# Kernel optimization log

Hardware: AMD Instinct MI355X
Metric: run time of the kernel (lower is better)

Reference implementation:

```python
import jax, jax.numpy as jnp
import numpy as np

N, IN_F, OUT_F, H = 4096, 128, 64, 8


def setup_inputs() -> dict:
    key = jax.random.key(0)
    k1, k2, k3, k4 = jax.random.split(key, 4)
    input_A = jax.random.normal(k1, (N, IN_F), jnp.float32)
    # linear_proj.weight: [H*OUT_F, IN_F] (torch Linear convention), xavier-ish scale
    Wp = jax.random.normal(k2, (H * OUT_F, IN_F), jnp.float32) * (1.0 / np.sqrt(IN_F))
    a_src = jax.random.normal(k3, (H, OUT_F), jnp.float32) * 0.1
    a_tgt = jax.random.normal(k4, (H, OUT_F), jnp.float32) * 0.1
    # dense additive mask (0 = connected); zeros => fully-connected graph, same math path
    adj_mask = jnp.zeros((N, N), jnp.float32)
    return {"input_A": input_A, "adj_mask": adj_mask, "Wp": Wp, "a_src": a_src, "a_tgt": a_tgt}


def reference(input_A, adj_mask, Wp, a_src, a_tgt):
    # dropout is identity in eval mode
    xp = (input_A @ Wp.T).reshape(-1, H, OUT_F)          # [N, H, F]
    ss = jnp.einsum('nhf,hf->hn', xp, a_src)             # scores_source, [H, N]
    st = jnp.einsum('nhf,hf->hn', xp, a_tgt)             # scores_target, [H, N]
    scores = jax.nn.leaky_relu(ss[:, :, None] + st[:, None, :], negative_slope=0.2)  # [H, N, N]
    attn = jax.nn.softmax(scores + adj_mask[None, :, :], axis=-1)                    # [H, N, N]
    out = jnp.einsum('hnm,mhf->nhf', attn, xp)           # bmm aggregate, [N, H, F]
    out = out.mean(axis=1)                               # mean over heads, [N, F]
    return jax.nn.relu(out)
```

## Files before the change

kernel.cpp:

```cpp
#include <hip/hip_runtime.h>
#include <hip/hip_bf16.h>
#include <cstdint>

#define GN 4096
#define GIN 128
#define GF 64
#define GH 8
#define GHF (GH*GF)
#define LOG2E 1.4426950408889634f

typedef __attribute__((ext_vector_type(8))) short short8v;
typedef __attribute__((ext_vector_type(4))) float f32x4;

__device__ __forceinline__ short f2bf(float x) {
    uint32_t u = __float_as_uint(x);
    uint32_t r = u + 0x7fffu + ((u >> 16) & 1u);
    return (short)(r >> 16);
}
__device__ __forceinline__ uint32_t pack_bf16_rh(float lo, float hi) {
    uint32_t a = __float_as_uint(lo) + 0x8000u;
    uint32_t b = __float_as_uint(hi) + 0x8000u;
    return __builtin_amdgcn_perm(b, a, 0x07060302u);
}
__device__ __forceinline__ float leaky(float t) { return fmaxf(t, 0.2f * t); }

__global__ void gat_zeroflag(uint32_t* __restrict__ f) {
    if (threadIdx.x == 0 && blockIdx.x == 0) f[0] = 0u;
}
__global__ __launch_bounds__(256) void gat_maskscan(const uint32_t* __restrict__ m,
                                                    uint32_t* __restrict__ flag) {
    uint32_t acc = 0;
    const uint4* m4 = (const uint4*)m;
    const int total = (GN * GN) / 4;
    for (int i = blockIdx.x * 256 + threadIdx.x; i < total; i += gridDim.x * 256) {
        uint4 v = m4[i];
        acc |= v.x | v.y | v.z | v.w;
    }
#pragma unroll
    for (int d = 1; d < 64; d <<= 1) acc |= (uint32_t)__shfl_xor((int)acc, d);
    __shared__ uint32_t wred[4];
    if ((threadIdx.x & 63) == 0) wred[threadIdx.x >> 6] = acc;
    __syncthreads();
    if (threadIdx.x == 0) {
        uint32_t a = wred[0] | wred[1] | wred[2] | wred[3];
        if (a) atomicOr(flag, 1u);
    }
}

__global__ __launch_bounds__(256) void gat_proj(const float* __restrict__ A,
                                                const float* __restrict__ W,
                                                const float* __restrict__ a_src,
                                                const float* __restrict__ a_tgt,
                                                float* __restrict__ ss,
                                                float* __restrict__ st,
                                                short* __restrict__ bh) {
    __shared__ float lds[2 * 64 * 129];
    float* As = lds;
    float* Ws = lds + 64 * 129;
    const int n0 = blockIdx.x * 64;
    const int h  = blockIdx.y;
    const int j0 = h * 64;
    const int tid = threadIdx.x;
    const float4* A4 = (const float4*)A;
    const float4* W4 = (const float4*)W;
#pragma unroll
    for (int i = 0; i < 8; ++i) {
        int idx = tid + i * 256;
        int r = idx >> 5, c4 = idx & 31;
        float4 v = A4[(size_t)(n0 + r) * 32 + c4];
        As[r * 129 + c4 * 4 + 0] = v.x; As[r * 129 + c4 * 4 + 1] = v.y;
        As[r * 129 + c4 * 4 + 2] = v.z; As[r * 129 + c4 * 4 + 3] = v.w;
        float4 w = W4[(size_t)(j0 + r) * 32 + c4];
        Ws[r * 129 + c4 * 4 + 0] = w.x; Ws[r * 129 + c4 * 4 + 1] = w.y;
        Ws[r * 129 + c4 * 4 + 2] = w.z; Ws[r * 129 + c4 * 4 + 3] = w.w;
    }
    __syncthreads();
    const int tx = tid & 15, ty = tid >> 4;
    float acc[4][4] = {};
    for (int k = 0; k < 128; ++k) {
        float a[4], b[4];
#pragma unroll
        for (int i = 0; i < 4; ++i) { a[i] = As[(ty * 4 + i) * 129 + k]; b[i] = Ws[(tx * 4 + i) * 129 + k]; }
#pragma unroll
        for (int i = 0; i < 4; ++i)
#pragma unroll
            for (int j = 0; j < 4; ++j) acc[i][j] = fmaf(a[i], b[j], acc[i][j]);
    }
    __syncthreads();
    float* X = lds;
#pragma unroll
    for (int i = 0; i < 4; ++i)
#pragma unroll
        for (int j = 0; j < 4; ++j)
            X[(ty * 4 + i) * 65 + tx * 4 + j] = acc[i][j];
    __syncthreads();

    const int lane = tid & 63, w = tid >> 6;
    float s1 = 0.f, s2 = 0.f;
#pragma unroll
    for (int k = 0; k < 16; ++k) {
        int f = w * 16 + k;
        float x = X[lane * 65 + f];
        s1 = fmaf(x, a_src[j0 + f], s1);
        s2 = fmaf(x, a_tgt[j0 + f], s2);
    }
    float* ps = lds + 64 * 129;
    ps[w * 64 + lane] = s1;
    ps[(4 + w) * 64 + lane] = s2;
    __syncthreads();
    if (w == 0) {
        ss[h * GN + n0 + lane] = ps[lane] + ps[64 + lane] + ps[128 + lane] + ps[192 + lane];
        st[h * GN + n0 + lane] = ps[256 + lane] + ps[320 + lane] + ps[384 + lane] + ps[448 + lane];
    }

#pragma unroll
    for (int rep = 0; rep < 2; ++rep) {
        int fid = tid + rep * 256;
        int t_local = fid >> 8, cf = (fid >> 6) & 3, lf = fid & 63;
        int gg = lf >> 4, c = lf & 15;
        short8v vh;
#pragma unroll
        for (int jj = 0; jj < 8; ++jj)
            vh[jj] = f2bf(X[(t_local * 32 + gg * 8 + jj) * 65 + cf * 16 + c]);
        ((short8v*)bh)[((size_t)(h * 128 + (n0 >> 5) + t_local) * 4 + cf) * 64 + lf] = vh;
    }
}

__global__ __launch_bounds__(256) void gat_stmax(const float* __restrict__ st,
                                                 float* __restrict__ stmax) {
    const int h = blockIdx.x;
    const int tid = threadIdx.x;
    float m = -1e30f;
    for (int i = tid; i < GN; i += 256) m = fmaxf(m, st[h * GN + i]);
#pragma unroll
    for (int d = 1; d < 64; d <<= 1) m = fmaxf(m, __shfl_xor(m, d));
    __shared__ float wred[4];
    if ((tid & 63) == 0) wred[tid >> 6] = m;
    __syncthreads();
    if (tid == 0)
        stmax[h] = fmaxf(fmaxf(wred[0], wred[1]), fmaxf(wred[2], wred[3]));
}

__global__ __launch_bounds__(256) void gat_attn_fast(const short* __restrict__ bh,
                                                     const float* __restrict__ ss,
                                                     const float* __restrict__ st,
                                                     const float* __restrict__ stmax,
                                                     const uint32_t* __restrict__ mflag,
                                                     float* __restrict__ acc_p,
                                                     float* __restrict__ l_p,
                                                     int S) {
    if (mflag[0] != 0u) return;
    const int lane = threadIdx.x & 63;
    const int h = blockIdx.y * 4 + (threadIdx.x >> 6);
    const int q0 = blockIdx.x * 64;
    const int s = blockIdx.z;
    const int TPS = 128 / S;
    const int g = lane >> 4;
    const int c = lane & 15;

    const float smx = stmax[h];
    float KP[4], KN[4];
#pragma unroll
    for (int qf = 0; qf < 4; ++qf) {
        float ssa = ss[h * GN + q0 + qf * 16 + c];
        float caL = leaky(ssa + smx) * LOG2E;
        KP[qf] = fmaf(ssa, LOG2E, -caL);
        KN[qf] = fmaf(0.2f * ssa, LOG2E, -caL);
    }

    const short BONE = (short)0x3F80;
    const short8v BONES = {BONE, BONE, BONE, BONE, BONE, BONE, BONE, BONE};

    f32x4 acc[4][4];
    f32x4 accL[4];
#pragma unroll
    for (int qf = 0; qf < 4; ++qf) {
        accL[qf] = (f32x4){0.f, 0.f, 0.f, 0.f};
#pragma unroll
        for (int cf = 0; cf < 4; ++cf) acc[qf][cf] = (f32x4){0.f, 0.f, 0.f, 0.f};
    }

    const int t0 = s * TPS;
    const float4* stp = (const float4*)&st[h * GN + t0 * 32 + g * 8];
    const short8v* bhp = (const short8v*)bh + ((size_t)(h * 128 + t0) * 4) * 64 + lane;

    float4 sA[2]; short8v HA[4];
    float4 sB[2]; short8v HB[4];

#define LOADT(sv, Hv) do {                                      \
    sv[0] = stp[0]; sv[1] = stp[1]; stp += 8;                   \
    _Pragma("unroll")                                           \
    for (int i = 0; i < 4; ++i) Hv[i] = bhp[i * 64];            \
    bhp += 256; } while (0)

#define COMPUTET(sv, Hv) do {                                               \
    float stvL[8] = {sv[0].x * LOG2E, sv[0].y * LOG2E, sv[0].z * LOG2E,     \
                     sv[0].w * LOG2E, sv[1].x * LOG2E, sv[1].y * LOG2E,     \
                     sv[1].z * LOG2E, sv[1].w * LOG2E};                     \
    _Pragma("unroll")                                                       \
    for (int qf = 0; qf < 4; ++qf) {                                        \
        float pa[8];                                                        \
        _Pragma("unroll")                                                   \
        for (int j = 0; j < 8; ++j) {                                       \
            float ea = fmaxf(stvL[j] + KP[qf], fmaf(stvL[j], 0.2f, KN[qf])); \
            pa[j] = __builtin_amdgcn_exp2f(ea);                             \
        }                                                                   \
        union { uint32_t u[4]; short8v v; } P;                              \
        _Pragma("unroll")                                                   \
        for (int w2 = 0; w2 < 4; ++w2)                                      \
            P.u[w2] = pack_bf16_rh(pa[2 * w2], pa[2 * w2 + 1]);             \
        _Pragma("unroll")                                                   \
        for (int cf = 0; cf < 4; ++cf)                                      \
            acc[qf][cf] = __builtin_amdgcn_mfma_f32_16x16x32_bf16(P.v, Hv[cf], acc[qf][cf], 0, 0, 0); \
        accL[qf] = __builtin_amdgcn_mfma_f32_16x16x32_bf16(P.v, BONES, accL[qf], 0, 0, 0); \
    } } while (0)

    LOADT(sA, HA);
    for (int t = 0; t + 2 < TPS; t += 2) {
        LOADT(sB, HB);
        COMPUTET(sA, HA);
        LOADT(sA, HA);
        COMPUTET(sB, HB);
    }
    LOADT(sB, HB);
    COMPUTET(sA, HA);
    COMPUTET(sB, HB);

#undef LOADT
#undef COMPUTET

    if (c == 0) {
#pragma unroll
        for (int qf = 0; qf < 4; ++qf)
#pragma unroll
            for (int r = 0; r < 4; ++r)
                l_p[(size_t)(s * GH + h) * GN + q0 + qf * 16 + g * 4 + r] = accL[qf][r];
    }
#pragma unroll
    for (int qf = 0; qf < 4; ++qf)
#pragma unroll
        for (int cf = 0; cf < 4; ++cf)
#pragma unroll
            for (int r = 0; r < 4; ++r)
                acc_p[((size_t)(s * GH + h) * GN + q0 + qf * 16 + g * 4 + r) * GF + cf * 16 + c]
                    = acc[qf][cf][r];
}

__global__ __launch_bounds__(256) void gat_attn_mask(const short* __restrict__ bh,
                                                     const float* __restrict__ ss,
                                                     const float* __restrict__ st,
                                                     const float* __restrict__ stmax,
                                                     const float* __restrict__ mask,
                                                     const uint32_t* __restrict__ mflag,
                                                     float* __restrict__ acc_p,
                                                     float* __restrict__ l_p,
                                                     int S) {
    if (mflag[0] == 0u) return;
    const int lane = threadIdx.x & 63;
    const int h = blockIdx.y * 4 + (threadIdx.x >> 6);
    const int q0 = blockIdx.x * 16;
    const int s = blockIdx.z;
    const int TPS = 128 / S;
    const int g = lane >> 4;

    const int qa = q0 + (lane & 15);
    const float ssa = ss[h * GN + qa];
    const float smx = stmax[h];
    const float caL = leaky(ssa + smx) * LOG2E;
    const float KaP = fmaf(ssa, LOG2E, -caL), KaN = fmaf(0.2f * ssa, LOG2E, -caL);

    const short BONE = (short)0x3F80;
    const short8v BONES = {BONE, BONE, BONE, BONE, BONE, BONE, BONE, BONE};

    f32x4 acc[4];
#pragma unroll
    for (int cf = 0; cf < 4; ++cf) acc[cf] = (f32x4){0.f, 0.f, 0.f, 0.f};
    f32x4 accL = (f32x4){0.f, 0.f, 0.f, 0.f};

    const int t0 = s * TPS;
    const float4* stp = (const float4*)&st[h * GN + t0 * 32 + g * 8];
    const float4* mpa = (const float4*)&mask[(size_t)qa * GN + t0 * 32 + g * 8];
    const short8v* bhp = (const short8v*)bh + ((size_t)(h * 128 + t0) * 4) * 64 + lane;

    for (int t = 0; t < TPS; ++t) {
        float4 s0 = stp[0], s1 = stp[1]; stp += 8;
        float4 a0 = mpa[0], a1 = mpa[1]; mpa += 8;
        short8v H[4];
#pragma unroll
        for (int i = 0; i < 4; ++i) H[i] = bhp[i * 64];
        bhp += 256;
        float stv[8] = {s0.x, s0.y, s0.z, s0.w, s1.x, s1.y, s1.z, s1.w};
        float mav[8] = {a0.x, a0.y, a0.z, a0.w, a1.x, a1.y, a1.z, a1.w};
        float pa[8];
#pragma unroll
        for (int j = 0; j < 8; ++j) {
            float stvL = stv[j] * LOG2E;
            float ea = fmaxf(stvL + KaP, fmaf(stvL, 0.2f, KaN));
            ea = fmaf(mav[j], LOG2E, ea);
            pa[j] = __builtin_amdgcn_exp2f(ea);
        }
        union { uint32_t u[4]; short8v v; } P;
#pragma unroll
        for (int w2 = 0; w2 < 4; ++w2) P.u[w2] = pack_bf16_rh(pa[2 * w2], pa[2 * w2 + 1]);
#pragma unroll
        for (int cf = 0; cf < 4; ++cf)
            acc[cf] = __builtin_amdgcn_mfma_f32_16x16x32_bf16(P.v, H[cf], acc[cf], 0, 0, 0);
        accL = __builtin_amdgcn_mfma_f32_16x16x32_bf16(P.v, BONES, accL, 0, 0, 0);
    }

    if ((lane & 15) == 0) {
#pragma unroll
        for (int r = 0; r < 4; ++r)
            l_p[(size_t)(s * GH + h) * GN + q0 + g * 4 + r] = accL[r];
    }
#pragma unroll
    for (int cf = 0; cf < 4; ++cf)
#pragma unroll
        for (int r = 0; r < 4; ++r)
            acc_p[((size_t)(s * GH + h) * GN + q0 + g * 4 + r) * GF + cf * 16 + (lane & 15)]
                = acc[cf][r];
}

__global__ __launch_bounds__(256) void gat_combine(const float* __restrict__ acc_p,
                                                   const float* __restrict__ l_p,
                                                   float* __restrict__ out, int S) {
    const int idx = blockIdx.x * 256 + threadIdx.x;
    const int n = idx >> 4, f4 = idx & 15;
    const float4* ap = (const float4*)acc_p;
    float4 r = {0.f, 0.f, 0.f, 0.f};
#pragma unroll
    for (int h = 0; h < GH; ++h) {
        float4 a = {0.f, 0.f, 0.f, 0.f};
        float l = 0.f;
        for (int s = 0; s < S; ++s) {
            float4 v = ap[((size_t)(s * GH + h) * GN + n) * 16 + f4];
            a.x += v.x; a.y += v.y; a.z += v.z; a.w += v.w;
            l += l_p[(size_t)(s * GH + h) * GN + n];
        }
        float il = 1.0f / l;
        r.x += a.x * il; r.y += a.y * il; r.z += a.z * il; r.w += a.w * il;
    }
    float4 o;
    o.x = fmaxf(r.x * 0.125f, 0.f);
    o.y = fmaxf(r.y * 0.125f, 0.f);
    o.z = fmaxf(r.z * 0.125f, 0.f);
    o.w = fmaxf(r.w * 0.125f, 0.f);
    ((float4*)out)[idx] = o;
}

extern "C" void kernel_launch(void* const* d_in, const int* in_sizes, int n_in,
                              void* d_out, int out_size, void* d_ws, size_t ws_size,
                              hipStream_t stream) {
    const float* A     = (const float*)d_in[0];
    const float* mask  = (const float*)d_in[1];
    const float* Wp    = (const float*)d_in[2];
    const float* a_src = (const float*)d_in[3];
    const float* a_tgt = (const float*)d_in[4];
    float* out = (float*)d_out;

    char* w = (char*)d_ws;
    float* ss    = (float*)w;              w += (size_t)GH * GN * 4;
    float* st    = (float*)w;              w += (size_t)GH * GN * 4;
    float* stmx  = (float*)w;              w += 256;
    uint32_t* mflag = (uint32_t*)w;        w += 256;
    short* bh    = (short*)w;              w += (size_t)GH * 128 * 4 * 64 * 8 * 2;
    size_t base = (size_t)(w - (char*)d_ws);
    size_t per_s = (size_t)GH * GN * GF * 4 + (size_t)GH * GN * 4;
    int S = 4;
    while (S > 1 && base + (size_t)S * per_s > ws_size) S >>= 1;
    float* acc_p = (float*)w;              w += (size_t)S * GH * GN * GF * 4;
    float* l_p   = (float*)w;

    gat_zeroflag<<<1, 64, 0, stream>>>(mflag);
    gat_maskscan<<<2048, 256, 0, stream>>>((const uint32_t*)mask, mflag);
    gat_proj<<<dim3(GN / 64, GH), 256, 0, stream>>>(A, Wp, a_src, a_tgt, ss, st, bh);
    gat_stmax<<<GH, 256, 0, stream>>>(st, stmx);
    gat_attn_fast<<<dim3(GN / 64, 2, S), 256, 0, stream>>>(bh, ss, st, stmx,
                                                           mflag, acc_p, l_p, S);
    gat_attn_mask<<<dim3(GN / 16, 2, S), 256, 0, stream>>>(bh, ss, st, stmx, mask,
                                                           mflag, acc_p, l_p, S);
    gat_combine<<<(GN * 16) / 256, 256, 0, stream>>>(acc_p, l_p, out, S);
}
```

Measured before the change: 90.50 us.

## Factor exp of leaky-relu scores into separable products and fuse mask scan into projection

The attention kernel now uses exp(max(a,b)) = max(exp(a), exp(b)) and splits each exponent into a per-source factor times a per-target factor. This replaces per-element exp2 calls with per-tile exp2 on the target scores plus multiplies and a max, cutting transcendental work in the inner loop. Separately, the standalone mask-scan kernel is removed and its OR-reduction over the mask is folded into the projection kernel's tail, saving a launch. Precomputing the factors risks overflow or underflow when scores are large, since the exponent is no longer bounded by the combined max.

```diff
diff --git a/kernel.cpp b/kernel.cpp
--- a/kernel.cpp
+++ b/kernel.cpp
@@ -27,33 +27,16 @@
 __global__ void gat_zeroflag(uint32_t* __restrict__ f) {
     if (threadIdx.x == 0 && blockIdx.x == 0) f[0] = 0u;
 }
-__global__ __launch_bounds__(256) void gat_maskscan(const uint32_t* __restrict__ m,
-                                                    uint32_t* __restrict__ flag) {
-    uint32_t acc = 0;
-    const uint4* m4 = (const uint4*)m;
-    const int total = (GN * GN) / 4;
-    for (int i = blockIdx.x * 256 + threadIdx.x; i < total; i += gridDim.x * 256) {
-        uint4 v = m4[i];
-        acc |= v.x | v.y | v.z | v.w;
-    }
-#pragma unroll
-    for (int d = 1; d < 64; d <<= 1) acc |= (uint32_t)__shfl_xor((int)acc, d);
-    __shared__ uint32_t wred[4];
-    if ((threadIdx.x & 63) == 0) wred[threadIdx.x >> 6] = acc;
-    __syncthreads();
-    if (threadIdx.x == 0) {
-        uint32_t a = wred[0] | wred[1] | wred[2] | wred[3];
-        if (a) atomicOr(flag, 1u);
-    }
-}
 
 __global__ __launch_bounds__(256) void gat_proj(const float* __restrict__ A,
                                                 const float* __restrict__ W,
                                                 const float* __restrict__ a_src,
                                                 const float* __restrict__ a_tgt,
+                                                const uint32_t* __restrict__ maskbits,
                                                 float* __restrict__ ss,
                                                 float* __restrict__ st,
-                                                short* __restrict__ bh) {
+                                                short* __restrict__ bh,
+                                                uint32_t* __restrict__ mflag) {
     __shared__ float lds[2 * 64 * 129];
     float* As = lds;
     float* Ws = lds + 64 * 129;
@@ -124,6 +107,19 @@
             vh[jj] = f2bf(X[(t_local * 32 + gg * 8 + jj) * 65 + cf * 16 + c]);
         ((short8v*)bh)[((size_t)(h * 128 + (n0 >> 5) + t_local) * 4 + cf) * 64 + lf] = vh;
     }
+
+    uint32_t accOr = 0;
+    const uint4* m4 = (const uint4*)maskbits;
+    const int nblocks = gridDim.x * gridDim.y;
+    const int bid = blockIdx.y * gridDim.x + blockIdx.x;
+    const int total = (GN * GN) / 4;
+    for (int i = bid * 256 + tid; i < total; i += nblocks * 256) {
+        uint4 v = m4[i];
+        accOr |= v.x | v.y | v.z | v.w;
+    }
+#pragma unroll
+    for (int d = 1; d < 64; d <<= 1) accOr |= (uint32_t)__shfl_xor((int)accOr, d);
+    if ((tid & 63) == 0 && accOr) atomicOr(mflag, 1u);
 }
 
 __global__ __launch_bounds__(256) void gat_stmax(const float* __restrict__ st,
@@ -159,13 +155,13 @@
     const int c = lane & 15;
 
     const float smx = stmax[h];
-    float KP[4], KN[4];
+    float EP[4], EN[4];
 #pragma unroll
     for (int qf = 0; qf < 4; ++qf) {
         float ssa = ss[h * GN + q0 + qf * 16 + c];
         float caL = leaky(ssa + smx) * LOG2E;
-        KP[qf] = fmaf(ssa, LOG2E, -caL);
-        KN[qf] = fmaf(0.2f * ssa, LOG2E, -caL);
+        EP[qf] = __builtin_amdgcn_exp2f(fmaf(ssa, LOG2E, -caL));
+        EN[qf] = __builtin_amdgcn_exp2f(fmaf(0.2f * ssa, LOG2E, -caL));
     }
 
     const short BONE = (short)0x3F80;
@@ -197,14 +193,18 @@
     float stvL[8] = {sv[0].x * LOG2E, sv[0].y * LOG2E, sv[0].z * LOG2E,     \
                      sv[0].w * LOG2E, sv[1].x * LOG2E, sv[1].y * LOG2E,     \
                      sv[1].z * LOG2E, sv[1].w * LOG2E};                     \
+    float e1[8], e2[8];                                                     \
+    _Pragma("unroll")                                                       \
+    for (int j = 0; j < 8; ++j) {                                           \
+        e1[j] = __builtin_amdgcn_exp2f(stvL[j]);                            \
+        e2[j] = __builtin_amdgcn_exp2f(0.2f * stvL[j]);                     \
+    }                                                                       \
     _Pragma("unroll")                                                       \
     for (int qf = 0; qf < 4; ++qf) {                                        \
         float pa[8];                                                        \
         _Pragma("unroll")                                                   \
-        for (int j = 0; j < 8; ++j) {                                       \
-            float ea = fmaxf(stvL[j] + KP[qf], fmaf(stvL[j], 0.2f, KN[qf])); \
-            pa[j] = __builtin_amdgcn_exp2f(ea);                             \
-        }                                                                   \
+        for (int j = 0; j < 8; ++j)                                         \
+            pa[j] = fmaxf(e1[j] * EP[qf], e2[j] * EN[qf]);                  \
         union { uint32_t u[4]; short8v v; } P;                              \
         _Pragma("unroll")                                                   \
         for (int w2 = 0; w2 < 4; ++w2)                                      \
@@ -372,8 +372,9 @@
     float* l_p   = (float*)w;
 
     gat_zeroflag<<<1, 64, 0, stream>>>(mflag);
-    gat_maskscan<<<2048, 256, 0, stream>>>((const uint32_t*)mask, mflag);
-    gat_proj<<<dim3(GN / 64, GH), 256, 0, stream>>>(A, Wp, a_src, a_tgt, ss, st, bh);
+    gat_proj<<<dim3(GN / 64, GH), 256, 0, stream>>>(A, Wp, a_src, a_tgt,
+                                                    (const uint32_t*)mask,
+                                                    ss, st, bh, mflag);
     gat_stmax<<<GH, 256, 0, stream>>>(st, stmx);
     gat_attn_fast<<<dim3(GN / 64, 2, S), 256, 0, stream>>>(bh, ss, st, stmx,
                                                            mflag, acc_p, l_p, S);
```

Measured after the change: 83.86 us. 7.3% less time.
